# Optimization experiments

Measured on AMD Instinct MI355X. Metric: run time of the kernel, lower is better.

## Reference

```python
import jax, jax.numpy as jnp
import numpy as np

N_USERS = 100_000
N_ITEMS = 50_000
N_EDGES = 2_000_000
D = 64
ALPHA = 0.5      # tanh-blend coefficient (alpha)
NORM_2 = -1.0    # exponent on back-aggregation degree norm (args.norm_2)


def setup_inputs() -> dict:
    key = jax.random.key(0)
    k1, k2, k3, k4, k5 = jax.random.split(key, 5)
    return {
        "h_user": jax.random.normal(k1, (N_USERS, D), jnp.float32) * 0.1,
        "pretrained_feature": jax.random.normal(k2, (N_ITEMS, D), jnp.float32),
        "edge_w": jax.random.normal(k3, (N_ITEMS, 1), jnp.float32),
        "src_idx": jax.random.randint(k4, (N_EDGES,), 0, N_USERS, dtype=jnp.int32),
        "dst_idx": jax.random.randint(k5, (N_EDGES,), 0, N_ITEMS, dtype=jnp.int32),
    }


def reference(h_user, pretrained_feature, edge_w, src_idx, dst_idx):
    # HGCNLayer.forward: bidirectional copy_src+sum aggregation with degree norm,
    # tanh prompt blend and node-softmax edge weighting.
    ones = jnp.ones((N_EDGES,), h_user.dtype)

    # forward pass user -> item: rst[d] = sum_{(s,d) in E} h_user[s]
    rst = jax.ops.segment_sum(h_user[src_idx], dst_idx, num_segments=N_ITEMS)  # [N_ITEMS, D]
    deg_dst = jnp.clip(jax.ops.segment_sum(ones, dst_idx, num_segments=N_ITEMS), 1.0)

    # alpha * tanh prompt blend
    rst = rst + ALPHA * jnp.tanh(pretrained_feature)
    # edge-prompt softmax scaling (softmax over nodes; see notes)
    rst = jax.nn.softmax(edge_w, axis=0) * rst
    # in-degree^-1 normalization
    rst = rst / deg_dst[:, None]

    # backward pass item -> user: bsrc[s] = sum_{(s,d) in E} rst[d]
    bsrc = jax.ops.segment_sum(rst[dst_idx], src_idx, num_segments=N_USERS)  # [N_USERS, D]
    deg_src = jnp.clip(jax.ops.segment_sum(ones, src_idx, num_segments=N_USERS), 1.0)
    bsrc = bsrc * jnp.power(deg_src, NORM_2)[:, None]
    return bsrc
```

## Files before the change

### kernel.cpp

```cpp
#include <hip/hip_runtime.h>
#include <hip/hip_bf16.h>
#include <math.h>

#define N_USERS 100000
#define N_ITEMS 50000
#define N_EDGES 2000000
#define D 64

#define FB_BINS 98
#define BB_BINS 196
#define NBINS   (FB_BINS + BB_BINS)
#define CHUNK   2048
#define NCHUNK  ((N_EDGES + CHUNK - 1) / CHUNK)
#define FWD_WGS 782
#define BWD_WGS 1563
#define CAP     4032

__device__ __forceinline__ float blo(unsigned u) {
    union { unsigned i; float f; } c; c.i = u << 16; return c.f;
}
__device__ __forceinline__ float bhi(unsigned u) {
    union { unsigned i; float f; } c; c.i = u & 0xFFFF0000u; return c.f;
}
__device__ __forceinline__ unsigned bpack(float x, float y) {
    __hip_bfloat16 a = __float2bfloat16(x), b = __float2bfloat16(y);
    unsigned short ua = *reinterpret_cast<unsigned short*>(&a);
    unsigned short ub = *reinterpret_cast<unsigned short*>(&b);
    return (unsigned)ua | ((unsigned)ub << 16);
}

__global__ __launch_bounds__(256) void h2b_kernel(
    const float2* __restrict__ in, unsigned* __restrict__ out, int n) {
    int stride = gridDim.x * blockDim.x;
    for (int i = blockIdx.x * blockDim.x + threadIdx.x; i < n; i += stride) {
        float2 v = in[i];
        out[i] = bpack(v.x, v.y);
    }
}

__global__ __launch_bounds__(256) void hist_kernel(
    const int* __restrict__ src, const int* __restrict__ dst, int* __restrict__ gh) {
    __shared__ int h[NBINS];
    for (int i = threadIdx.x; i < NBINS; i += 256) h[i] = 0;
    __syncthreads();
    int stride = gridDim.x * blockDim.x;
    for (int e = blockIdx.x * blockDim.x + threadIdx.x; e < N_EDGES; e += stride) {
        atomicAdd(&h[dst[e] >> 9], 1);
        atomicAdd(&h[FB_BINS + (src[e] >> 9)], 1);
    }
    __syncthreads();
    for (int i = threadIdx.x; i < NBINS; i += 256) {
        int v = h[i];
        if (v) atomicAdd(&gh[i], v);
    }
}

__global__ void scan_excl(const int* __restrict__ in, int* __restrict__ out,
                          int* __restrict__ cur, int n) {
    const int T = 1024, E = 4;
    __shared__ int wsum[16];
    __shared__ int s_carry;
    if (threadIdx.x == 0) s_carry = 0;
    __syncthreads();

    int lane = threadIdx.x & 63;
    int wid  = threadIdx.x >> 6;

    for (int base = 0; base < n; base += T * E) {
        int idx0 = base + threadIdx.x * E;
        int v[E];
        int tot = 0;
#pragma unroll
        for (int e = 0; e < E; e++) {
            int i = idx0 + e;
            v[e] = (i < n) ? in[i] : 0;
            tot += v[e];
        }
        int incl = tot;
#pragma unroll
        for (int off = 1; off < 64; off <<= 1) {
            int t = __shfl_up(incl, off);
            if (lane >= off) incl += t;
        }
        if (lane == 63) wsum[wid] = incl;
        __syncthreads();
        if (wid == 0 && lane < 16) {
            int t = wsum[lane];
            int sc = t;
#pragma unroll
            for (int off = 1; off < 16; off <<= 1) {
                int u = __shfl_up(sc, off);
                if (lane >= off) sc += u;
            }
            wsum[lane] = sc - t;
        }
        __syncthreads();
        int wave_off = wsum[wid];
        int excl = s_carry + wave_off + incl - tot;
#pragma unroll
        for (int e = 0; e < E; e++) {
            int i = idx0 + e;
            if (i < n) { out[i] = excl; cur[i] = excl; }
            excl += v[e];
        }
        __syncthreads();
        if (threadIdx.x == T - 1) s_carry += wave_off + incl;
        __syncthreads();
    }
    if (threadIdx.x == 0) out[n] = s_carry;
}

__global__ __launch_bounds__(256) void binfill_kernel(
    const int* __restrict__ src, const int* __restrict__ dst,
    int* __restrict__ gcur, unsigned* __restrict__ stage) {
    __shared__ int cnt[NBINS];
    __shared__ int gbase[NBINS];
    __shared__ int lcur[NBINS];
    int c = blockIdx.x;
    int base = c * CHUNK;
    int nEdge = N_EDGES - base; if (nEdge > CHUNK) nEdge = CHUNK;

    for (int t = threadIdx.x; t < NBINS; t += 256) { cnt[t] = 0; lcur[t] = 0; }
    __syncthreads();

    int es[8], ed[8];
#pragma unroll
    for (int j = 0; j < 8; j++) {
        int k = j * 256 + threadIdx.x;
        if (k < nEdge) {
            es[j] = src[base + k];
            ed[j] = dst[base + k];
            atomicAdd(&cnt[ed[j] >> 9], 1);
            atomicAdd(&cnt[FB_BINS + (es[j] >> 9)], 1);
        } else {
            es[j] = -1;
        }
    }
    __syncthreads();
    for (int t = threadIdx.x; t < NBINS; t += 256) {
        int cv = cnt[t];
        gbase[t] = cv ? atomicAdd(&gcur[t], cv) : 0;
    }
    __syncthreads();
#pragma unroll
    for (int j = 0; j < 8; j++) {
        if (es[j] >= 0) {
            int s = es[j], d = ed[j];
            int bf = d >> 9;
            int p = atomicAdd(&lcur[bf], 1);
            stage[gbase[bf] + p] = (unsigned)s | ((unsigned)(d & 511) << 17);
            int bb = FB_BINS + (s >> 9);
            int q = atomicAdd(&lcur[bb], 1);
            stage[gbase[bb] + q] = (unsigned)d | ((unsigned)(s & 511) << 16);
        }
    }
}

__global__ void softmax_stats_kernel(const float* __restrict__ w, float* __restrict__ stats) {
    __shared__ float red[16];
    int tid = threadIdx.x, lane = tid & 63, wid = tid >> 6;

    float m = -INFINITY;
    for (int i = tid; i < N_ITEMS; i += 1024) m = fmaxf(m, w[i]);
#pragma unroll
    for (int off = 32; off; off >>= 1) m = fmaxf(m, __shfl_xor(m, off));
    if (lane == 0) red[wid] = m;
    __syncthreads();
    if (tid == 0) {
        float t = red[0];
        for (int k = 1; k < 16; k++) t = fmaxf(t, red[k]);
        red[0] = t;
    }
    __syncthreads();
    m = red[0];
    __syncthreads();

    float s = 0.f;
    for (int i = tid; i < N_ITEMS; i += 1024) s += expf(w[i] - m);
#pragma unroll
    for (int off = 32; off; off >>= 1) s += __shfl_xor(s, off);
    if (lane == 0) red[wid] = s;
    __syncthreads();
    if (tid == 0) {
        float t = 0.f;
        for (int k = 0; k < 16; k++) t += red[k];
        stats[0] = m;
        stats[1] = t;
    }
}

__global__ __launch_bounds__(512) void pass2_fwd_kernel(
    const unsigned* __restrict__ hu16, const float* __restrict__ pf,
    const float* __restrict__ edge_w, const unsigned* __restrict__ stage,
    const int* __restrict__ binoff, const float* __restrict__ stats,
    unsigned* __restrict__ rst16) {
    __shared__ int cnt[64];
    __shared__ int loc[65];
    __shared__ int lcur[64];
    __shared__ int sorted[CAP];
    int r = blockIdx.x;
    int B = r >> 3, sub = r & 7;
    int beg = binoff[B], end = binoff[B + 1];
    int tid = threadIdx.x, lane = tid & 63, wv = tid >> 6;
    int q = lane & 31, half = lane >> 5;

    if (tid < 64) { cnt[tid] = 0; lcur[tid] = 0; }
    __syncthreads();

    for (int k = beg + tid; k < end; k += 512) {
        unsigned e = stage[k];
        if ((int)(e >> 23) == sub) atomicAdd(&cnt[(e >> 17) & 63], 1);
    }
    __syncthreads();
    if (tid < 64) {
        int v = cnt[tid];
        int incl = v;
#pragma unroll
        for (int off = 1; off < 64; off <<= 1) {
            int t = __shfl_up(incl, off);
            if (tid >= off) incl += t;
        }
        loc[tid] = incl - v;
        if (tid == 63) loc[64] = incl;
    }
    __syncthreads();
    int nf = loc[64];

    float m = stats[0], ssum = stats[1];
    const float2* PF2 = (const float2*)pf;

    if (nf <= CAP) {
        for (int k = beg + tid; k < end; k += 512) {
            unsigned e = stage[k];
            if ((int)(e >> 23) == sub) {
                int il = (e >> 17) & 63;
                int p = atomicAdd(&lcur[il], 1);
                sorted[loc[il] + p] = (int)(e & 0x1FFFFu);
            }
        }
        __syncthreads();
        for (int il = wv; il < 64; il += 8) {
            int i = r * 64 + il;
            if (i >= N_ITEMS) continue;
            int a = loc[il], b = loc[il + 1];
            float ax = 0.f, ay = 0.f;
            int k = a;
            for (; k + 8 <= b; k += 8) {
                int s0 = sorted[k + half],     s1 = sorted[k + 2 + half];
                int s2 = sorted[k + 4 + half], s3 = sorted[k + 6 + half];
                unsigned u0 = hu16[(s0 << 5) + q];
                unsigned u1 = hu16[(s1 << 5) + q];
                unsigned u2 = hu16[(s2 << 5) + q];
                unsigned u3 = hu16[(s3 << 5) + q];
                ax += (blo(u0) + blo(u1)) + (blo(u2) + blo(u3));
                ay += (bhi(u0) + bhi(u1)) + (bhi(u2) + bhi(u3));
            }
            for (; k + 2 <= b; k += 2) {
                unsigned u = hu16[(sorted[k + half] << 5) + q];
                ax += blo(u); ay += bhi(u);
            }
            if (k < b && half == 0) {
                unsigned u = hu16[(sorted[k] << 5) + q];
                ax += blo(u); ay += bhi(u);
            }
            ax += __shfl_xor(ax, 32);
            ay += __shfl_xor(ay, 32);
            if (half == 0) {
                float deg = (float)(b - a);
                if (deg < 1.f) deg = 1.f;
                float sc = expf(edge_w[i] - m) / (ssum * deg);
                float2 pv = PF2[(size_t)i * 32 + q];
                float vx = (ax + 0.5f * tanhf(pv.x)) * sc;
                float vy = (ay + 0.5f * tanhf(pv.y)) * sc;
                rst16[(size_t)i * 32 + q] = bpack(vx, vy);
            }
        }
    } else {
        const unsigned short* HU = (const unsigned short*)hu16;
        for (int il = wv; il < 64; il += 8) {
            int i = r * 64 + il;
            if (i >= N_ITEMS) continue;
            unsigned want = ((unsigned)sub << 6) | (unsigned)il;
            float acc = 0.f;
            int dcount = 0;
            for (int k = beg; k < end; k++) {
                unsigned e = stage[k];
                if ((e >> 17) == want) {
                    union { unsigned u; float f; } c;
                    c.u = (unsigned)HU[(size_t)(e & 0x1FFFFu) * 64 + lane] << 16;
                    acc += c.f; dcount++;
                }
            }
            float deg = (float)dcount;
            if (deg < 1.f) deg = 1.f;
            float sc = expf(edge_w[i] - m) / (ssum * deg);
            float val = (acc + 0.5f * tanhf(pf[(size_t)i * D + lane])) * sc;
            float va = __shfl(val, 2 * q);
            float vb = __shfl(val, 2 * q + 1);
            if (half == 0) rst16[(size_t)i * 32 + q] = bpack(va, vb);
        }
    }
}

__global__ __launch_bounds__(512) void pass2_bwd_kernel(
    const unsigned* __restrict__ rst16, const unsigned* __restrict__ stage,
    const int* __restrict__ binoff, float* __restrict__ out) {
    __shared__ int cnt[64];
    __shared__ int loc[65];
    __shared__ int lcur[64];
    __shared__ int sorted[CAP];
    int r = blockIdx.x;
    int B = FB_BINS + (r >> 3), sub = r & 7;
    int beg = binoff[B], end = binoff[B + 1];
    int tid = threadIdx.x, lane = tid & 63, wv = tid >> 6;
    int q = lane & 31, half = lane >> 5;

    if (tid < 64) { cnt[tid] = 0; lcur[tid] = 0; }
    __syncthreads();

    for (int k = beg + tid; k < end; k += 512) {
        unsigned e = stage[k];
        if ((int)(e >> 22) == sub) atomicAdd(&cnt[(e >> 16) & 63], 1);
    }
    __syncthreads();
    if (tid < 64) {
        int v = cnt[tid];
        int incl = v;
#pragma unroll
        for (int off = 1; off < 64; off <<= 1) {
            int t = __shfl_up(incl, off);
            if (tid >= off) incl += t;
        }
        loc[tid] = incl - v;
        if (tid == 63) loc[64] = incl;
    }
    __syncthreads();
    int nf = loc[64];

    float2* OUT2 = (float2*)out;

    if (nf <= CAP) {
        for (int k = beg + tid; k < end; k += 512) {
            unsigned e = stage[k];
            if ((int)(e >> 22) == sub) {
                int il = (e >> 16) & 63;
                int p = atomicAdd(&lcur[il], 1);
                sorted[loc[il] + p] = (int)(e & 0xFFFFu);
            }
        }
        __syncthreads();
        for (int il = wv; il < 64; il += 8) {
            int u = r * 64 + il;
            if (u >= N_USERS) continue;
            int a = loc[il], b = loc[il + 1];
            float ax = 0.f, ay = 0.f;
            int k = a;
            for (; k + 8 <= b; k += 8) {
                int d0 = sorted[k + half],     d1 = sorted[k + 2 + half];
                int d2 = sorted[k + 4 + half], d3 = sorted[k + 6 + half];
                unsigned u0 = rst16[(d0 << 5) + q];
                unsigned u1 = rst16[(d1 << 5) + q];
                unsigned u2 = rst16[(d2 << 5) + q];
                unsigned u3 = rst16[(d3 << 5) + q];
                ax += (blo(u0) + blo(u1)) + (blo(u2) + blo(u3));
                ay += (bhi(u0) + bhi(u1)) + (bhi(u2) + bhi(u3));
            }
            for (; k + 2 <= b; k += 2) {
                unsigned e = rst16[(sorted[k + half] << 5) + q];
                ax += blo(e); ay += bhi(e);
            }
            if (k < b && half == 0) {
                unsigned e = rst16[(sorted[k] << 5) + q];
                ax += blo(e); ay += bhi(e);
            }
            ax += __shfl_xor(ax, 32);
            ay += __shfl_xor(ay, 32);
            if (half == 0) {
                float deg = (float)(b - a);
                if (deg < 1.f) deg = 1.f;
                OUT2[(size_t)u * 32 + q] = make_float2(ax / deg, ay / deg);
            }
        }
    } else {
        const unsigned short* RS = (const unsigned short*)rst16;
        for (int il = wv; il < 64; il += 8) {
            int u = r * 64 + il;
            if (u >= N_USERS) continue;
            unsigned want = ((unsigned)sub << 6) | (unsigned)il;
            float acc = 0.f;
            int dcount = 0;
            for (int k = beg; k < end; k++) {
                unsigned e = stage[k];
                if ((e >> 16) == want) {
                    union { unsigned ui; float f; } c;
                    c.ui = (unsigned)RS[(size_t)(e & 0xFFFFu) * 64 + lane] << 16;
                    acc += c.f; dcount++;
                }
            }
            float deg = (float)dcount;
            if (deg < 1.f) deg = 1.f;
            out[(size_t)u * D + lane] = acc / deg;
        }
    }
}

extern "C" void kernel_launch(void* const* d_in, const int* in_sizes, int n_in,
                              void* d_out, int out_size, void* d_ws, size_t ws_size,
                              hipStream_t stream) {
    const float* h_user = (const float*)d_in[0];
    const float* pf     = (const float*)d_in[1];
    const float* edge_w = (const float*)d_in[2];
    const int*   src    = (const int*)d_in[3];
    const int*   dst    = (const int*)d_in[4];
    float* out = (float*)d_out;

    char* p = (char*)d_ws;
    int* gh     = (int*)p;      p += sizeof(int) * NBINS;
    int* binoff = (int*)p;      p += sizeof(int) * (NBINS + 1);
    int* gcur   = (int*)p;      p += sizeof(int) * NBINS;
    unsigned* stage = (unsigned*)p; p += sizeof(unsigned) * (size_t)2 * N_EDGES;
    unsigned* hu16  = (unsigned*)p; p += sizeof(unsigned) * (size_t)N_USERS * 32;
    unsigned* rst16 = (unsigned*)p; p += sizeof(unsigned) * (size_t)N_ITEMS * 32;
    float* stats = (float*)p;   p += 2 * sizeof(float);

    hipMemsetAsync(gh, 0, sizeof(int) * NBINS, stream);

    hist_kernel<<<256, 256, 0, stream>>>(src, dst, gh);
    scan_excl<<<1, 1024, 0, stream>>>(gh, binoff, gcur, NBINS);
    binfill_kernel<<<NCHUNK, 256, 0, stream>>>(src, dst, gcur, stage);
    h2b_kernel<<<1024, 256, 0, stream>>>((const float2*)h_user, hu16, N_USERS * 32);
    softmax_stats_kernel<<<1, 1024, 0, stream>>>(edge_w, stats);
    pass2_fwd_kernel<<<FWD_WGS, 512, 0, stream>>>(hu16, pf, edge_w, stage, binoff, stats, rst16);
    pass2_bwd_kernel<<<BWD_WGS, 512, 0, stream>>>(rst16, stage, binoff, out);
}
```

Before: 347.2 us.

## Build per-node CSR with a counting-sort pass instead of per-block bin rescans

New measurement: 350.2 us. No clear change (+0.9%).

```diff
diff --git a/kernel.cpp b/kernel.cpp
--- a/kernel.cpp
+++ b/kernel.cpp
@@ -12,9 +12,10 @@
 #define NBINS   (FB_BINS + BB_BINS)
 #define CHUNK   2048
 #define NCHUNK  ((N_EDGES + CHUNK - 1) / CHUNK)
-#define FWD_WGS 782
-#define BWD_WGS 1563
-#define CAP     4032
+#define FINE_FWD (FB_BINS * 512)
+#define FINE_ALL (FINE_FWD + BB_BINS * 512)
+#define FWD_WGS ((N_ITEMS + 31) / 32)
+#define BWD_WGS ((N_USERS + 31) / 32)
 
 __device__ __forceinline__ float blo(unsigned u) {
     union { unsigned i; float f; } c; c.i = u << 16; return c.f;
@@ -156,6 +157,54 @@
     }
 }
 
+__global__ __launch_bounds__(512) void redist_kernel(
+    const unsigned* __restrict__ stage, const int* __restrict__ binoff,
+    unsigned* __restrict__ stage2, int* __restrict__ fineoff) {
+    __shared__ int cnt[512];
+    __shared__ int wsum[8];
+    int B = blockIdx.x;
+    int fwd = (B < FB_BINS) ? 1 : 0;
+    int beg = binoff[B], end = binoff[B + 1];
+    int tid = threadIdx.x, lane = tid & 63, wv = tid >> 6;
+    int sh = fwd ? 17 : 16;
+    unsigned pmask = fwd ? 0x1FFFFu : 0xFFFFu;
+
+    cnt[tid] = 0;
+    __syncthreads();
+    for (int k = beg + tid; k < end; k += 512)
+        atomicAdd(&cnt[(stage[k] >> sh) & 511], 1);
+    __syncthreads();
+
+    int v = cnt[tid];
+    int incl = v;
+#pragma unroll
+    for (int off = 1; off < 64; off <<= 1) {
+        int t = __shfl_up(incl, off);
+        if (lane >= off) incl += t;
+    }
+    if (lane == 63) wsum[wv] = incl;
+    __syncthreads();
+    if (tid == 0) {
+        int run = 0;
+#pragma unroll
+        for (int w = 0; w < 8; w++) { int t = wsum[w]; wsum[w] = run; run += t; }
+    }
+    __syncthreads();
+    int excl = wsum[wv] + incl - v;
+
+    int fbase = fwd ? (B * 512) : (FINE_FWD + (B - FB_BINS) * 512);
+    fineoff[fbase + tid] = beg + excl;
+    cnt[tid] = excl;
+    __syncthreads();
+
+    for (int k = beg + tid; k < end; k += 512) {
+        unsigned e = stage[k];
+        int lid = (e >> sh) & 511;
+        int p = atomicAdd(&cnt[lid], 1);
+        stage2[beg + p] = e & pmask;
+    }
+}
+
 __global__ void softmax_stats_kernel(const float* __restrict__ w, float* __restrict__ stats) {
     __shared__ float red[16];
     int tid = threadIdx.x, lane = tid & 63, wid = tid >> 6;
@@ -189,217 +238,93 @@
     }
 }
 
-__global__ __launch_bounds__(512) void pass2_fwd_kernel(
+__global__ __launch_bounds__(256) void pass2_fwd_kernel(
     const unsigned* __restrict__ hu16, const float* __restrict__ pf,
-    const float* __restrict__ edge_w, const unsigned* __restrict__ stage,
-    const int* __restrict__ binoff, const float* __restrict__ stats,
+    const float* __restrict__ edge_w, const unsigned* __restrict__ stage2,
+    const int* __restrict__ fineoff, const float* __restrict__ stats,
     unsigned* __restrict__ rst16) {
-    __shared__ int cnt[64];
-    __shared__ int loc[65];
-    __shared__ int lcur[64];
-    __shared__ int sorted[CAP];
-    int r = blockIdx.x;
-    int B = r >> 3, sub = r & 7;
-    int beg = binoff[B], end = binoff[B + 1];
     int tid = threadIdx.x, lane = tid & 63, wv = tid >> 6;
     int q = lane & 31, half = lane >> 5;
-
-    if (tid < 64) { cnt[tid] = 0; lcur[tid] = 0; }
-    __syncthreads();
-
-    for (int k = beg + tid; k < end; k += 512) {
-        unsigned e = stage[k];
-        if ((int)(e >> 23) == sub) atomicAdd(&cnt[(e >> 17) & 63], 1);
-    }
-    __syncthreads();
-    if (tid < 64) {
-        int v = cnt[tid];
-        int incl = v;
-#pragma unroll
-        for (int off = 1; off < 64; off <<= 1) {
-            int t = __shfl_up(incl, off);
-            if (tid >= off) incl += t;
-        }
-        loc[tid] = incl - v;
-        if (tid == 63) loc[64] = incl;
-    }
-    __syncthreads();
-    int nf = loc[64];
-
     float m = stats[0], ssum = stats[1];
     const float2* PF2 = (const float2*)pf;
-
-    if (nf <= CAP) {
-        for (int k = beg + tid; k < end; k += 512) {
-            unsigned e = stage[k];
-            if ((int)(e >> 23) == sub) {
-                int il = (e >> 17) & 63;
-                int p = atomicAdd(&lcur[il], 1);
-                sorted[loc[il] + p] = (int)(e & 0x1FFFFu);
-            }
-        }
-        __syncthreads();
-        for (int il = wv; il < 64; il += 8) {
-            int i = r * 64 + il;
-            if (i >= N_ITEMS) continue;
-            int a = loc[il], b = loc[il + 1];
-            float ax = 0.f, ay = 0.f;
-            int k = a;
-            for (; k + 8 <= b; k += 8) {
-                int s0 = sorted[k + half],     s1 = sorted[k + 2 + half];
-                int s2 = sorted[k + 4 + half], s3 = sorted[k + 6 + half];
-                unsigned u0 = hu16[(s0 << 5) + q];
-                unsigned u1 = hu16[(s1 << 5) + q];
-                unsigned u2 = hu16[(s2 << 5) + q];
-                unsigned u3 = hu16[(s3 << 5) + q];
-                ax += (blo(u0) + blo(u1)) + (blo(u2) + blo(u3));
-                ay += (bhi(u0) + bhi(u1)) + (bhi(u2) + bhi(u3));
-            }
-            for (; k + 2 <= b; k += 2) {
-                unsigned u = hu16[(sorted[k + half] << 5) + q];
-                ax += blo(u); ay += bhi(u);
-            }
-            if (k < b && half == 0) {
-                unsigned u = hu16[(sorted[k] << 5) + q];
-                ax += blo(u); ay += bhi(u);
-            }
-            ax += __shfl_xor(ax, 32);
-            ay += __shfl_xor(ay, 32);
-            if (half == 0) {
-                float deg = (float)(b - a);
-                if (deg < 1.f) deg = 1.f;
-                float sc = expf(edge_w[i] - m) / (ssum * deg);
-                float2 pv = PF2[(size_t)i * 32 + q];
-                float vx = (ax + 0.5f * tanhf(pv.x)) * sc;
-                float vy = (ay + 0.5f * tanhf(pv.y)) * sc;
-                rst16[(size_t)i * 32 + q] = bpack(vx, vy);
-            }
-        }
-    } else {
-        const unsigned short* HU = (const unsigned short*)hu16;
-        for (int il = wv; il < 64; il += 8) {
-            int i = r * 64 + il;
-            if (i >= N_ITEMS) continue;
-            unsigned want = ((unsigned)sub << 6) | (unsigned)il;
-            float acc = 0.f;
-            int dcount = 0;
-            for (int k = beg; k < end; k++) {
-                unsigned e = stage[k];
-                if ((e >> 17) == want) {
-                    union { unsigned u; float f; } c;
-                    c.u = (unsigned)HU[(size_t)(e & 0x1FFFFu) * 64 + lane] << 16;
-                    acc += c.f; dcount++;
-                }
-            }
-            float deg = (float)dcount;
+    int i0 = blockIdx.x * 32;
+
+    for (int il = wv; il < 32; il += 4) {
+        int i = i0 + il;
+        if (i >= N_ITEMS) break;
+        int a = fineoff[i], b = fineoff[i + 1];
+        float ax = 0.f, ay = 0.f;
+        int k = a;
+        for (; k + 8 <= b; k += 8) {
+            int s0 = (int)stage2[k + half],     s1 = (int)stage2[k + 2 + half];
+            int s2 = (int)stage2[k + 4 + half], s3 = (int)stage2[k + 6 + half];
+            unsigned u0 = hu16[(s0 << 5) + q];
+            unsigned u1 = hu16[(s1 << 5) + q];
+            unsigned u2 = hu16[(s2 << 5) + q];
+            unsigned u3 = hu16[(s3 << 5) + q];
+            ax += (blo(u0) + blo(u1)) + (blo(u2) + blo(u3));
+            ay += (bhi(u0) + bhi(u1)) + (bhi(u2) + bhi(u3));
+        }
+        for (; k + 2 <= b; k += 2) {
+            unsigned u = hu16[((int)stage2[k + half] << 5) + q];
+            ax += blo(u); ay += bhi(u);
+        }
+        if (k < b && half == 0) {
+            unsigned u = hu16[((int)stage2[k] << 5) + q];
+            ax += blo(u); ay += bhi(u);
+        }
+        ax += __shfl_xor(ax, 32);
+        ay += __shfl_xor(ay, 32);
+        if (half == 0) {
+            float deg = (float)(b - a);
             if (deg < 1.f) deg = 1.f;
             float sc = expf(edge_w[i] - m) / (ssum * deg);
-            float val = (acc + 0.5f * tanhf(pf[(size_t)i * D + lane])) * sc;
-            float va = __shfl(val, 2 * q);
-            float vb = __shfl(val, 2 * q + 1);
-            if (half == 0) rst16[(size_t)i * 32 + q] = bpack(va, vb);
-        }
-    }
-}
-
-__global__ __launch_bounds__(512) void pass2_bwd_kernel(
-    const unsigned* __restrict__ rst16, const unsigned* __restrict__ stage,
-    const int* __restrict__ binoff, float* __restrict__ out) {
-    __shared__ int cnt[64];
-    __shared__ int loc[65];
-    __shared__ int lcur[64];
-    __shared__ int sorted[CAP];
-    int r = blockIdx.x;
-    int B = FB_BINS + (r >> 3), sub = r & 7;
-    int beg = binoff[B], end = binoff[B + 1];
+            float2 pv = PF2[(size_t)i * 32 + q];
+            float vx = (ax + 0.5f * tanhf(pv.x)) * sc;
+            float vy = (ay + 0.5f * tanhf(pv.y)) * sc;
+            rst16[(size_t)i * 32 + q] = bpack(vx, vy);
+        }
+    }
+}
+
+__global__ __launch_bounds__(256) void pass2_bwd_kernel(
+    const unsigned* __restrict__ rst16, const unsigned* __restrict__ stage2,
+    const int* __restrict__ fineoff, float* __restrict__ out) {
     int tid = threadIdx.x, lane = tid & 63, wv = tid >> 6;
     int q = lane & 31, half = lane >> 5;
-
-    if (tid < 64) { cnt[tid] = 0; lcur[tid] = 0; }
-    __syncthreads();
-
-    for (int k = beg + tid; k < end; k += 512) {
-        unsigned e = stage[k];
-        if ((int)(e >> 22) == sub) atomicAdd(&cnt[(e >> 16) & 63], 1);
-    }
-    __syncthreads();
-    if (tid < 64) {
-        int v = cnt[tid];
-        int incl = v;
-#pragma unroll
-        for (int off = 1; off < 64; off <<= 1) {
-            int t = __shfl_up(incl, off);
-            if (tid >= off) incl += t;
-        }
-        loc[tid] = incl - v;
-        if (tid == 63) loc[64] = incl;
-    }
-    __syncthreads();
-    int nf = loc[64];
-
     float2* OUT2 = (float2*)out;
-
-    if (nf <= CAP) {
-        for (int k = beg + tid; k < end; k += 512) {
-            unsigned e = stage[k];
-            if ((int)(e >> 22) == sub) {
-                int il = (e >> 16) & 63;
-                int p = atomicAdd(&lcur[il], 1);
-                sorted[loc[il] + p] = (int)(e & 0xFFFFu);
-            }
-        }
-        __syncthreads();
-        for (int il = wv; il < 64; il += 8) {
-            int u = r * 64 + il;
-            if (u >= N_USERS) continue;
-            int a = loc[il], b = loc[il + 1];
-            float ax = 0.f, ay = 0.f;
-            int k = a;
-            for (; k + 8 <= b; k += 8) {
-                int d0 = sorted[k + half],     d1 = sorted[k + 2 + half];
-                int d2 = sorted[k + 4 + half], d3 = sorted[k + 6 + half];
-                unsigned u0 = rst16[(d0 << 5) + q];
-                unsigned u1 = rst16[(d1 << 5) + q];
-                unsigned u2 = rst16[(d2 << 5) + q];
-                unsigned u3 = rst16[(d3 << 5) + q];
-                ax += (blo(u0) + blo(u1)) + (blo(u2) + blo(u3));
-                ay += (bhi(u0) + bhi(u1)) + (bhi(u2) + bhi(u3));
-            }
-            for (; k + 2 <= b; k += 2) {
-                unsigned e = rst16[(sorted[k + half] << 5) + q];
-                ax += blo(e); ay += bhi(e);
-            }
-            if (k < b && half == 0) {
-                unsigned e = rst16[(sorted[k] << 5) + q];
-                ax += blo(e); ay += bhi(e);
-            }
-            ax += __shfl_xor(ax, 32);
-            ay += __shfl_xor(ay, 32);
-            if (half == 0) {
-                float deg = (float)(b - a);
-                if (deg < 1.f) deg = 1.f;
-                OUT2[(size_t)u * 32 + q] = make_float2(ax / deg, ay / deg);
-            }
-        }
-    } else {
-        const unsigned short* RS = (const unsigned short*)rst16;
-        for (int il = wv; il < 64; il += 8) {
-            int u = r * 64 + il;
-            if (u >= N_USERS) continue;
-            unsigned want = ((unsigned)sub << 6) | (unsigned)il;
-            float acc = 0.f;
-            int dcount = 0;
-            for (int k = beg; k < end; k++) {
-                unsigned e = stage[k];
-                if ((e >> 16) == want) {
-                    union { unsigned ui; float f; } c;
-                    c.ui = (unsigned)RS[(size_t)(e & 0xFFFFu) * 64 + lane] << 16;
-                    acc += c.f; dcount++;
-                }
-            }
-            float deg = (float)dcount;
+    int u0i = blockIdx.x * 32;
+
+    for (int il = wv; il < 32; il += 4) {
+        int u = u0i + il;
+        if (u >= N_USERS) break;
+        int a = fineoff[FINE_FWD + u], b = fineoff[FINE_FWD + u + 1];
+        float ax = 0.f, ay = 0.f;
+        int k = a;
+        for (; k + 8 <= b; k += 8) {
+            int d0 = (int)stage2[k + half],     d1 = (int)stage2[k + 2 + half];
+            int d2 = (int)stage2[k + 4 + half], d3 = (int)stage2[k + 6 + half];
+            unsigned u0 = rst16[(d0 << 5) + q];
+            unsigned u1 = rst16[(d1 << 5) + q];
+            unsigned u2 = rst16[(d2 << 5) + q];
+            unsigned u3 = rst16[(d3 << 5) + q];
+            ax += (blo(u0) + blo(u1)) + (blo(u2) + blo(u3));
+            ay += (bhi(u0) + bhi(u1)) + (bhi(u2) + bhi(u3));
+        }
+        for (; k + 2 <= b; k += 2) {
+            unsigned e = rst16[((int)stage2[k + half] << 5) + q];
+            ax += blo(e); ay += bhi(e);
+        }
+        if (k < b && half == 0) {
+            unsigned e = rst16[((int)stage2[k] << 5) + q];
+            ax += blo(e); ay += bhi(e);
+        }
+        ax += __shfl_xor(ax, 32);
+        ay += __shfl_xor(ay, 32);
+        if (half == 0) {
+            float deg = (float)(b - a);
             if (deg < 1.f) deg = 1.f;
-            out[(size_t)u * D + lane] = acc / deg;
+            OUT2[(size_t)u * 32 + q] = make_float2(ax / deg, ay / deg);
         }
     }
 }
@@ -415,21 +340,24 @@
     float* out = (float*)d_out;
 
     char* p = (char*)d_ws;
-    int* gh     = (int*)p;      p += sizeof(int) * NBINS;
-    int* binoff = (int*)p;      p += sizeof(int) * (NBINS + 1);
-    int* gcur   = (int*)p;      p += sizeof(int) * NBINS;
-    unsigned* stage = (unsigned*)p; p += sizeof(unsigned) * (size_t)2 * N_EDGES;
-    unsigned* hu16  = (unsigned*)p; p += sizeof(unsigned) * (size_t)N_USERS * 32;
-    unsigned* rst16 = (unsigned*)p; p += sizeof(unsigned) * (size_t)N_ITEMS * 32;
-    float* stats = (float*)p;   p += 2 * sizeof(float);
+    int* gh      = (int*)p;      p += sizeof(int) * NBINS;
+    int* binoff  = (int*)p;      p += sizeof(int) * (NBINS + 1);
+    int* gcur    = (int*)p;      p += sizeof(int) * NBINS;
+    int* fineoff = (int*)p;      p += sizeof(int) * FINE_ALL;
+    unsigned* stage  = (unsigned*)p; p += sizeof(unsigned) * (size_t)2 * N_EDGES;
+    unsigned* stage2 = (unsigned*)p; p += sizeof(unsigned) * (size_t)2 * N_EDGES;
+    unsigned* hu16   = (unsigned*)p; p += sizeof(unsigned) * (size_t)N_USERS * 32;
+    unsigned* rst16  = (unsigned*)p; p += sizeof(unsigned) * (size_t)N_ITEMS * 32;
+    float* stats = (float*)p;    p += 2 * sizeof(float);
 
     hipMemsetAsync(gh, 0, sizeof(int) * NBINS, stream);
 
     hist_kernel<<<256, 256, 0, stream>>>(src, dst, gh);
     scan_excl<<<1, 1024, 0, stream>>>(gh, binoff, gcur, NBINS);
     binfill_kernel<<<NCHUNK, 256, 0, stream>>>(src, dst, gcur, stage);
+    redist_kernel<<<NBINS, 512, 0, stream>>>(stage, binoff, stage2, fineoff);
     h2b_kernel<<<1024, 256, 0, stream>>>((const float2*)h_user, hu16, N_USERS * 32);
     softmax_stats_kernel<<<1, 1024, 0, stream>>>(edge_w, stats);
-    pass2_fwd_kernel<<<FWD_WGS, 512, 0, stream>>>(hu16, pf, edge_w, stage, binoff, stats, rst16);
-    pass2_bwd_kernel<<<BWD_WGS, 512, 0, stream>>>(rst16, stage, binoff, out);
-}
+    pass2_fwd_kernel<<<FWD_WGS, 256, 0, stream>>>(hu16, pf, edge_w, stage2, fineoff, stats, rst16);
+    pass2_bwd_kernel<<<BWD_WGS, 256, 0, stream>>>(rst16, stage2, fineoff, out);
+}
```
